# Performance work log

Hardware: AMD Instinct MI355X
Metric: run time of the kernel (lower is better)

## Reference

```python
import jax, jax.numpy as jnp
import numpy as np

EMB = 768
HEADS = 12
HEAD_DIM = EMB // HEADS
LN_EPS = 1e-5


def _layernorm(x, g, b):
    mu = jnp.mean(x, axis=-1, keepdims=True)
    var = jnp.mean(jnp.square(x - mu), axis=-1, keepdims=True)
    return (x - mu) * jax.lax.rsqrt(var + LN_EPS) * g + b


def _att_block(x, ln_g, ln_b, w_qkv, b_qkv, w_proj, b_proj):
    # x: [b, n, e]
    B, N, E = x.shape
    h, d = HEADS, HEAD_DIM
    qkv = _layernorm(x, ln_g, ln_b) @ w_qkv.T + b_qkv          # [b, n, 3e]
    # einops 'b n (h d qkv)': last axis factors as (h, d, 3), qkv innermost
    qkv = qkv.reshape(B, N, h, d, 3)
    qkv = jnp.moveaxis(qkv, (4, 2), (0, 2))                    # [3, b, h, n, d]
    q, k, v = qkv[0], qkv[1], qkv[2]
    scale = d ** (-0.5)
    # NOTE: original code DIVIDES by scale (= multiplies by sqrt(d)) -- faithful
    scores = jnp.einsum('bhqd,bhkd->bhqk', q, k) / scale       # [b, h, n, n]
    attn = jax.nn.softmax(scores, axis=-1)
    out = jnp.einsum('bhqk,bhkd->bhqd', attn, v)               # [b, h, n, d]
    out = out.transpose(0, 2, 1, 3).reshape(B, N, E)           # [b, n, e]
    return x + out @ w_proj.T + b_proj


def setup_inputs() -> dict:
    key = jax.random.key(0)
    ks = jax.random.split(key, 8)
    B, N, E = 2, 2048, EMB
    s = E ** (-0.5)
    return {
        'modal1': jax.random.normal(ks[0], (B, N, E), jnp.float32),
        'modal2': jax.random.normal(ks[1], (B, N, E), jnp.float32),
        'ln1_g': jnp.ones((E,), jnp.float32),
        'ln1_b': jnp.zeros((E,), jnp.float32),
        'w_qkv1': jax.random.normal(ks[2], (3 * E, E), jnp.float32) * s,
        'b_qkv1': jnp.zeros((3 * E,), jnp.float32),
        'w_proj1': jax.random.normal(ks[3], (E, E), jnp.float32) * s,
        'b_proj1': jnp.zeros((E,), jnp.float32),
        'ln2_g': jnp.ones((E,), jnp.float32),
        'ln2_b': jnp.zeros((E,), jnp.float32),
        'w_qkv2': jax.random.normal(ks[4], (3 * E, E), jnp.float32) * s,
        'b_qkv2': jnp.zeros((3 * E,), jnp.float32),
        'w_proj2': jax.random.normal(ks[5], (E, E), jnp.float32) * s,
        'b_proj2': jnp.zeros((E,), jnp.float32),
    }


def reference(modal1, modal2, ln1_g, ln1_b, w_qkv1, b_qkv1, w_proj1, b_proj1,
              ln2_g, ln2_b, w_qkv2, b_qkv2, w_proj2, b_proj2):
    out1 = _att_block(modal1, ln1_g, ln1_b, w_qkv1, b_qkv1, w_proj1, b_proj1)
    out2 = _att_block(modal2, ln2_g, ln2_b, w_qkv2, b_qkv2, w_proj2, b_proj2)
    return (out1, out2)
```

## Files before the change

### kernel.cpp

```cpp
#include <hip/hip_runtime.h>
#include <hip/hip_bf16.h>


typedef unsigned short u16;
typedef unsigned int   u32;
typedef __attribute__((ext_vector_type(4)))  float floatx4;
typedef __attribute__((ext_vector_type(16))) float floatx16;
typedef __attribute__((ext_vector_type(8)))  short shortx8;
typedef __attribute__((ext_vector_type(2)))  unsigned int uintx2;

#define EMB   768
#define SEQ   2048
#define NHEAD 12
#define HDIM  64
#define RPM   4096
#define NROW  8192
#define NUNIT 48
#define LDA   40
#define KTS   4096

__device__ __forceinline__ float bf2f(u16 h) {
  union { u32 u; float f; } v; v.u = ((u32)h) << 16; return v.f;
}
__device__ __forceinline__ u16 f2bf(float f) {
  union { float f; u32 u; } v; v.f = f;
  u32 r = v.u + 0x7fffu + ((v.u >> 16) & 1u);
  return (u16)(r >> 16);
}
__device__ __forceinline__ u32 cvtpk_bf16(float a, float b) {
  u32 r;
  asm("v_cvt_pk_bf16_f32 %0, %1, %2" : "=v"(r) : "v"(a), "v"(b));
  return r;
}
__device__ __forceinline__ void swap_halves(u32 a, u32 b, u32& x, u32& y) {
#if __has_builtin(__builtin_amdgcn_permlane32_swap)
  uintx2 r = __builtin_amdgcn_permlane32_swap(a, b, false, false);
  x = r.x; y = r.y;
#else
  u32 ax = (u32)__shfl_xor((int)a, 32);
  u32 bx = (u32)__shfl_xor((int)b, 32);
  bool h = (threadIdx.x & 32) != 0;
  x = h ? bx : a;
  y = h ? b : ax;
#endif
}

__global__ __launch_bounds__(256) void prep_wq(
    const float* __restrict__ wq1, const float* __restrict__ wq2,
    u16* __restrict__ wh, u16* __restrict__ wl)
{
  int bx = blockIdx.x;
  int modal = bx / 2304, rowp = bx % 2304;
  int typ = rowp / 768, hd = rowp % 768;
  const float* W = (modal ? wq2 : wq1) + (size_t)(hd * 3 + typ) * EMB;
  size_t dst = (size_t)bx * EMB;
  int t = threadIdx.x;
  #pragma unroll
  for (int i = 0; i < 3; ++i) {
    int e = t + i * 256;
    float v = W[e];
    u16 h = f2bf(v);
    wh[dst + e] = h;
    wl[dst + e] = f2bf(v - bf2f(h));
  }
}

__global__ __launch_bounds__(256) void prep_wp(
    const float* __restrict__ wp1, const float* __restrict__ wp2,
    u16* __restrict__ wh)
{
  int bx = blockIdx.x;
  int modal = bx / 768, row = bx % 768;
  const float* W = (modal ? wp2 : wp1) + (size_t)row * EMB;
  size_t dst = (size_t)bx * EMB;
  int t = threadIdx.x;
  #pragma unroll
  for (int i = 0; i < 3; ++i) {
    int e = t + i * 256;
    wh[dst + e] = f2bf(W[e]);
  }
}

__global__ __launch_bounds__(256) void k_ln(
    const float* __restrict__ x1, const float* __restrict__ x2,
    const float* __restrict__ g1, const float* __restrict__ b1,
    const float* __restrict__ g2, const float* __restrict__ b2,
    u16* __restrict__ xn_hi, u16* __restrict__ xn_lo)
{
  int row = blockIdx.x;
  int modal = row >> 12;
  const float* x = modal ? x2 : x1;
  const float* g = modal ? g2 : g1;
  const float* bb = modal ? b2 : b1;
  int r = row & (RPM - 1);
  const float* xr = x + (size_t)r * EMB;
  int t = threadIdx.x;
  float v0 = xr[t], v1 = xr[t + 256], v2 = xr[t + 512];
  float s = v0 + v1 + v2;
  float s2 = v0 * v0 + v1 * v1 + v2 * v2;
  #pragma unroll
  for (int m = 1; m < 64; m <<= 1) { s += __shfl_xor(s, m); s2 += __shfl_xor(s2, m); }
  __shared__ float ls[4], ls2[4];
  int w = t >> 6;
  if ((t & 63) == 0) { ls[w] = s; ls2[w] = s2; }
  __syncthreads();
  s = ls[0] + ls[1] + ls[2] + ls[3];
  s2 = ls2[0] + ls2[1] + ls2[2] + ls2[3];
  float mu = s * (1.0f / EMB);
  float var = s2 * (1.0f / EMB) - mu * mu;
  float rs = rsqrtf(var + 1e-5f);
  size_t base = (size_t)row * EMB;
  float vv[3] = { v0, v1, v2 };
  #pragma unroll
  for (int i = 0; i < 3; ++i) {
    int e = t + i * 256;
    float xn = (vv[i] - mu) * rs * g[e] + bb[e];
    u16 h = f2bf(xn);
    xn_hi[base + e] = h;
    xn_lo[base + e] = f2bf(xn - bf2f(h));
  }
}

__global__ __launch_bounds__(256) void k_qkv(
    const u16* __restrict__ xn_hi, const u16* __restrict__ xn_lo,
    const u16* __restrict__ wqh, const u16* __restrict__ wql,
    const float* __restrict__ bq1, const float* __restrict__ bq2,
    u16* __restrict__ q_hi, u16* __restrict__ q_lo,
    u16* __restrict__ k_hi, u16* __restrict__ k_lo,
    u16* __restrict__ vT)
{
  int mt = blockIdx.x, ntile = blockIdx.y, modal = blockIdx.z;
  const float* BQ = modal ? bq2 : bq1;
  int typ = ntile / 6;
  int hd0 = (ntile % 6) * 128;

  __shared__ u16 As_hi[128 * LDA], As_lo[128 * LDA], Wh[128 * LDA], Wl[128 * LDA];

  int tid = threadIdx.x, lane = tid & 63, w = tid >> 6;
  int wm = (w >> 1) * 64, wn = (w & 1) * 64;
  int lc = lane & 15, lq = lane >> 4;

  floatx4 acc[4][4] = {};
  size_t arow0 = (size_t)(modal * RPM + mt * 128) * EMB;
  size_t wrow0 = (size_t)(modal * 2304 + typ * 768 + hd0) * EMB;

  for (int k0 = 0; k0 < EMB; k0 += 32) {
    #pragma unroll
    for (int i = 0; i < 2; ++i) {
      int c = tid + i * 256;
      int rr = c >> 2, cc = (c & 3) * 8;
      size_t go = (size_t)rr * EMB + k0 + cc;
      *(shortx8*)&As_hi[rr * LDA + cc] = *(const shortx8*)(xn_hi + arow0 + go);
      *(shortx8*)&Wh[rr * LDA + cc]    = *(const shortx8*)(wqh + wrow0 + go);
      if (typ != 2) {
        *(shortx8*)&As_lo[rr * LDA + cc] = *(const shortx8*)(xn_lo + arow0 + go);
        *(shortx8*)&Wl[rr * LDA + cc]    = *(const shortx8*)(wql + wrow0 + go);
      }
    }
    __syncthreads();
    shortx8 ah[4], al[4], wh[4], wl[4];
    #pragma unroll
    for (int i = 0; i < 4; ++i) {
      ah[i] = *(const shortx8*)&As_hi[(wm + i * 16 + lc) * LDA + lq * 8];
      wh[i] = *(const shortx8*)&Wh[(wn + i * 16 + lc) * LDA + lq * 8];
      if (typ != 2) {
        al[i] = *(const shortx8*)&As_lo[(wm + i * 16 + lc) * LDA + lq * 8];
        wl[i] = *(const shortx8*)&Wl[(wn + i * 16 + lc) * LDA + lq * 8];
      }
    }
    #pragma unroll
    for (int i = 0; i < 4; ++i)
      #pragma unroll
      for (int jn = 0; jn < 4; ++jn) {
        acc[i][jn] = __builtin_amdgcn_mfma_f32_16x16x32_bf16(ah[i], wh[jn], acc[i][jn], 0, 0, 0);
        if (typ != 2) {
          acc[i][jn] = __builtin_amdgcn_mfma_f32_16x16x32_bf16(al[i], wh[jn], acc[i][jn], 0, 0, 0);
          acc[i][jn] = __builtin_amdgcn_mfma_f32_16x16x32_bf16(ah[i], wl[jn], acc[i][jn], 0, 0, 0);
        }
      }
    __syncthreads();
  }

  #pragma unroll
  for (int i = 0; i < 4; ++i) {
    int mrow0 = mt * 128 + wm + i * 16 + lq * 4;
    #pragma unroll
    for (int jn = 0; jn < 4; ++jn) {
      int colp = hd0 + wn + jn * 16 + lc;
      int h = colp >> 6, d = colp & 63;
      float bias = BQ[colp * 3 + typ];
      #pragma unroll
      for (int r = 0; r < 4; ++r) {
        int mrow = mrow0 + r;
        int b = mrow >> 11, nq = mrow & (SEQ - 1);
        int uu = modal * 24 + b * 12 + h;
        float val = acc[i][jn][r] + bias;
        if (typ == 0) {
          size_t o = ((size_t)uu * SEQ + nq) * HDIM + d;
          u16 hh = f2bf(val); q_hi[o] = hh; q_lo[o] = f2bf(val - bf2f(hh));
        } else if (typ == 1) {
          size_t o = ((size_t)uu * SEQ + nq) * HDIM + d;
          u16 hh = f2bf(val); k_hi[o] = hh; k_lo[o] = f2bf(val - bf2f(hh));
        } else {
          vT[((size_t)uu * HDIM + d) * SEQ + nq] = f2bf(val);
        }
      }
    }
  }
}

__global__ __launch_bounds__(256, 3) void k_attn(
    const u16* __restrict__ q_hi, const u16* __restrict__ q_lo,
    const u16* __restrict__ k_hi, const u16* __restrict__ k_lo,
    const u16* __restrict__ vT, u16* __restrict__ attn_out)
{
  int qt = blockIdx.x, u = blockIdx.y;
  __shared__ u16 lds[2][3 * KTS];

  int tid = threadIdx.x, lane = tid & 63, w = tid >> 6;
  int col = lane & 31, hi = lane >> 5;
  int swz = (col & 7) << 4;

  shortx8 qh[4], qlo[4];
  {
    size_t qb = ((size_t)u * SEQ + qt * 128 + w * 32 + col) * HDIM + hi * 8;
    #pragma unroll
    for (int s = 0; s < 4; ++s) {
      qh[s]  = *(const shortx8*)(q_hi + qb + s * 16);
      qlo[s] = *(const shortx8*)(q_lo + qb + s * 16);
    }
  }

  int lrow = lane >> 3;
  int lcol = ((lane & 7) ^ lrow) << 3;
  const u16* kh_src = k_hi + (size_t)u * SEQ * HDIM;
  const u16* kl_src = k_lo + (size_t)u * SEQ * HDIM;
  const u16* v_src  = vT  + (size_t)u * HDIM * SEQ;

  auto stage = [&](int buf, int kc) {
    #pragma unroll
    for (int c = 0; c < 6; ++c) {
      int seg = w * 6 + c;
      int tile = seg >> 3, segin = seg & 7;
      u16* dst = &lds[buf][tile * KTS + segin * 512];
      const u16* src;
      if (tile == 0)      src = kh_src + (size_t)(kc + segin * 8 + lrow) * HDIM + lcol;
      else if (tile == 1) src = kl_src + (size_t)(kc + segin * 8 + lrow) * HDIM + lcol;
      else                src = v_src  + (size_t)(segin * 8 + lrow) * SEQ + kc + lcol;
      __builtin_amdgcn_global_load_lds(
          (const __attribute__((address_space(1))) unsigned int*)src,
          (__attribute__((address_space(3))) unsigned int*)dst, 16, 0, 0);
    }
  };

  floatx16 O0 = {}, O1 = {};
  float m_r = -1e30f, lsum = 0.0f;
  const float Cs = 11.5415603271f;
  const float THR = 8.0f;

  stage(0, 0);
  __syncthreads();

  for (int t = 0; t < SEQ / 64; ++t) {
    int cur = t & 1;
    if (t + 1 < SEQ / 64) stage(cur ^ 1, (t + 1) * 64);

    const char* Kh = (const char*)&lds[cur][0];
    const char* Kl = (const char*)&lds[cur][KTS];
    const char* Vt = (const char*)&lds[cur][2 * KTS];

    floatx16 S0 = {}, S1 = {};
    __builtin_amdgcn_s_setprio(1);
    #pragma unroll
    for (int s = 0; s < 4; ++s) {
      int cb = (s * 32 + hi * 16) ^ swz;
      shortx8 kf0 = *(const shortx8*)(Kh + col * 128 + cb);
      shortx8 kl0 = *(const shortx8*)(Kl + col * 128 + cb);
      shortx8 kf1 = *(const shortx8*)(Kh + (32 + col) * 128 + cb);
      shortx8 kl1 = *(const shortx8*)(Kl + (32 + col) * 128 + cb);
      S0 = __builtin_amdgcn_mfma_f32_32x32x16_bf16(kf0, qh[s],  S0, 0, 0, 0);
      S1 = __builtin_amdgcn_mfma_f32_32x32x16_bf16(kf1, qh[s],  S1, 0, 0, 0);
      S0 = __builtin_amdgcn_mfma_f32_32x32x16_bf16(kf0, qlo[s], S0, 0, 0, 0);
      S1 = __builtin_amdgcn_mfma_f32_32x32x16_bf16(kf1, qlo[s], S1, 0, 0, 0);
      S0 = __builtin_amdgcn_mfma_f32_32x32x16_bf16(kl0, qh[s],  S0, 0, 0, 0);
      S1 = __builtin_amdgcn_mfma_f32_32x32x16_bf16(kl1, qh[s],  S1, 0, 0, 0);
    }
    __builtin_amdgcn_s_setprio(0);

    float tm[16];
    #pragma unroll
    for (int r = 0; r < 16; ++r) tm[r] = fmaxf(S0[r], S1[r]);
    #pragma unroll
    for (int st = 8; st >= 1; st >>= 1)
      #pragma unroll
      for (int i = 0; i < st; ++i) tm[i] = fmaxf(tm[i], tm[i + st]);
    float mx = tm[0] * Cs;
    mx = fmaxf(mx, __shfl_xor(mx, 32));

    if (!__all(mx <= m_r + THR)) {
      float mn = fmaxf(m_r, mx);
      float alpha = __builtin_amdgcn_exp2f(m_r - mn);
      m_r = mn;
      lsum *= alpha;
      #pragma unroll
      for (int r = 0; r < 16; ++r) {
        int qsrc = (r & 3) + 8 * (r >> 2) + 4 * hi;
        union { float f; int i; } a; a.f = alpha;
        a.i = __builtin_amdgcn_ds_bpermute(qsrc << 2, a.i);
        O0[r] *= a.f; O1[r] *= a.f;
      }
    }

    #pragma unroll
    for (int r = 0; r < 16; ++r) {
      S0[r] = __builtin_amdgcn_exp2f(fmaf(Cs, S0[r], -m_r));
      S1[r] = __builtin_amdgcn_exp2f(fmaf(Cs, S1[r], -m_r));
    }
    #pragma unroll
    for (int r = 0; r < 16; ++r) tm[r] = S0[r] + S1[r];
    #pragma unroll
    for (int st = 8; st >= 1; st >>= 1)
      #pragma unroll
      for (int i = 0; i < st; ++i) tm[i] += tm[i + st];
    lsum += tm[0];

    shortx8 pf[4];
    #pragma unroll
    for (int kt = 0; kt < 2; ++kt)
      #pragma unroll
      for (int h2 = 0; h2 < 2; ++h2) {
        floatx16 Sv = kt ? S1 : S0;
        int b0 = h2 * 8;
        u32 A = cvtpk_bf16(Sv[b0 + 0], Sv[b0 + 1]);
        u32 B = cvtpk_bf16(Sv[b0 + 2], Sv[b0 + 3]);
        u32 C = cvtpk_bf16(Sv[b0 + 4], Sv[b0 + 5]);
        u32 D = cvtpk_bf16(Sv[b0 + 6], Sv[b0 + 7]);
        u32 w0, w1, w2, w3;
        swap_halves(A, C, w0, w2);
        swap_halves(B, D, w1, w3);
        union { u32 uu[4]; shortx8 ss; } pk_;
        pk_.uu[0] = w0; pk_.uu[1] = w1; pk_.uu[2] = w2; pk_.uu[3] = w3;
        pf[kt * 2 + h2] = pk_.ss;
      }

    __builtin_amdgcn_s_setprio(1);
    #pragma unroll
    for (int ks = 0; ks < 4; ++ks) {
      int cb = (ks * 32 + hi * 16) ^ swz;
      shortx8 v0 = *(const shortx8*)(Vt + col * 128 + cb);
      shortx8 v1 = *(const shortx8*)(Vt + (32 + col) * 128 + cb);
      O0 = __builtin_amdgcn_mfma_f32_32x32x16_bf16(pf[ks], v0, O0, 0, 0, 0);
      O1 = __builtin_amdgcn_mfma_f32_32x32x16_bf16(pf[ks], v1, O1, 0, 0, 0);
    }
    __builtin_amdgcn_s_setprio(0);

    __syncthreads();
  }

  float lt = lsum + __shfl_xor(lsum, 32);
  float rl = __builtin_amdgcn_rcpf(lt);
  int modal = u / 24, b = (u / 12) & 1, h = u % 12;
  size_t obase = ((size_t)(modal * RPM + b * SEQ + qt * 128 + w * 32)) * EMB + h * 64 + col;
  #pragma unroll
  for (int r = 0; r < 16; ++r) {
    int ql_ = (r & 3) + 8 * (r >> 2) + 4 * hi;
    union { float f; int i; } a; a.f = rl;
    a.i = __builtin_amdgcn_ds_bpermute(ql_ << 2, a.i);
    size_t ob = obase + (size_t)ql_ * EMB;
    attn_out[ob]      = f2bf(O0[r] * a.f);
    attn_out[ob + 32] = f2bf(O1[r] * a.f);
  }
}

__global__ __launch_bounds__(256) void k_proj(
    const u16* __restrict__ ao, const u16* __restrict__ wph,
    const float* __restrict__ x1, const float* __restrict__ x2,
    const float* __restrict__ bp1, const float* __restrict__ bp2,
    float* __restrict__ out)
{
  int mt = blockIdx.x, ntile = blockIdx.y, modal = blockIdx.z;
  const float* BP = modal ? bp2 : bp1;
  const float* x  = modal ? x2 : x1;

  __shared__ u16 As[128 * LDA], Ws[128 * LDA];
  int tid = threadIdx.x, lane = tid & 63, w = tid >> 6;
  int wm = (w >> 1) * 64, wn = (w & 1) * 64;
  int lc = lane & 15, lq = lane >> 4;

  floatx4 acc[4][4] = {};
  size_t arow0 = (size_t)(modal * RPM + mt * 128) * EMB;
  int col0 = ntile * 128;
  size_t wrow0 = (size_t)(modal * 768 + col0) * EMB;

  for (int k0 = 0; k0 < EMB; k0 += 32) {
    #pragma unroll
    for (int i = 0; i < 2; ++i) {
      int c = tid + i * 256;
      int rr = c >> 2, cc = (c & 3) * 8;
      size_t go = (size_t)rr * EMB + k0 + cc;
      *(shortx8*)&As[rr * LDA + cc] = *(const shortx8*)(ao + arow0 + go);
      *(shortx8*)&Ws[rr * LDA + cc] = *(const shortx8*)(wph + wrow0 + go);
    }
    __syncthreads();
    shortx8 af[4], wf[4];
    #pragma unroll
    for (int i = 0; i < 4; ++i) {
      af[i] = *(const shortx8*)&As[(wm + i * 16 + lc) * LDA + lq * 8];
      wf[i] = *(const shortx8*)&Ws[(wn + i * 16 + lc) * LDA + lq * 8];
    }
    #pragma unroll
    for (int i = 0; i < 4; ++i)
      #pragma unroll
      for (int jn = 0; jn < 4; ++jn)
        acc[i][jn] = __builtin_amdgcn_mfma_f32_16x16x32_bf16(af[i], wf[jn], acc[i][jn], 0, 0, 0);
    __syncthreads();
  }

  #pragma unroll
  for (int i = 0; i < 4; ++i) {
    int mrow0 = mt * 128 + wm + i * 16 + lq * 4;
    #pragma unroll
    for (int jn = 0; jn < 4; ++jn) {
      int col = col0 + wn + jn * 16 + lc;
      float bias = BP[col];
      #pragma unroll
      for (int r = 0; r < 4; ++r) {
        int mrow = mrow0 + r;
        float val = acc[i][jn][r] + bias + x[(size_t)mrow * EMB + col];
        out[((size_t)(modal * RPM + mrow)) * EMB + col] = val;
      }
    }
  }
}

extern "C" void kernel_launch(void* const* d_in, const int* in_sizes, int n_in,
                              void* d_out, int out_size, void* d_ws, size_t ws_size,
                              hipStream_t stream) {
  const float* modal1 = (const float*)d_in[0];
  const float* modal2 = (const float*)d_in[1];
  const float* ln1_g  = (const float*)d_in[2];
  const float* ln1_b  = (const float*)d_in[3];
  const float* w_qkv1 = (const float*)d_in[4];
  const float* b_qkv1 = (const float*)d_in[5];
  const float* w_proj1= (const float*)d_in[6];
  const float* b_proj1= (const float*)d_in[7];
  const float* ln2_g  = (const float*)d_in[8];
  const float* ln2_b  = (const float*)d_in[9];
  const float* w_qkv2 = (const float*)d_in[10];
  const float* b_qkv2 = (const float*)d_in[11];
  const float* w_proj2= (const float*)d_in[12];
  const float* b_proj2= (const float*)d_in[13];
  float* out = (float*)d_out;

  const size_t BUFE = (size_t)NROW * EMB;
  const size_t WQE  = (size_t)2 * 2304 * EMB;
  u16* xn_hi = (u16*)d_ws;
  u16* xn_lo = xn_hi + BUFE;
  u16* q_hi  = xn_lo + BUFE;
  u16* q_lo  = q_hi + BUFE;
  u16* k_hi  = q_lo + BUFE;
  u16* k_lo  = k_hi + BUFE;
  u16* vT    = k_lo + BUFE;
  u16* wq_h  = vT + BUFE;
  u16* wq_l  = wq_h + WQE;
  u16* attn  = xn_hi;
  u16* wp_h  = q_lo;

  prep_wq<<<4608, 256, 0, stream>>>(w_qkv1, w_qkv2, wq_h, wq_l);
  k_ln<<<NROW, 256, 0, stream>>>(modal1, modal2, ln1_g, ln1_b, ln2_g, ln2_b, xn_hi, xn_lo);
  dim3 g2(32, 18, 2);
  k_qkv<<<g2, 256, 0, stream>>>(xn_hi, xn_lo, wq_h, wq_l, b_qkv1, b_qkv2,
                                q_hi, q_lo, k_hi, k_lo, vT);
  dim3 g3(16, 48);
  k_attn<<<g3, 256, 0, stream>>>(q_hi, q_lo, k_hi, k_lo, vT, attn);
  prep_wp<<<1536, 256, 0, stream>>>(w_proj1, w_proj2, wp_h);
  dim3 g4(32, 6, 2);
  k_proj<<<g4, 256, 0, stream>>>(attn, wp_h, modal1, modal2, b_proj1, b_proj2, out);
}
```

Before: 357.2 us.

## Double query rows per attention wave and use async LDS loads in QKV GEMM

The attention kernel now has each wave process two 32-row query groups against the same staged K/V tile. Each block covers 256 queries, the grid halves, and every K/V LDS fragment read is reused across twice as many MFMAs. This raises register pressure, so occupancy drops to 2 blocks per CU and only 384 blocks fill the device. The QKV GEMM switches from register-staged global-to-LDS copies to global_load_lds with an XOR-swizzled unpadded layout, and it skips the lo-part loads for V tiles.

```diff
diff --git a/kernel.cpp b/kernel.cpp
--- a/kernel.cpp
+++ b/kernel.cpp
@@ -134,48 +134,74 @@
   int typ = ntile / 6;
   int hd0 = (ntile % 6) * 128;
 
-  __shared__ u16 As_hi[128 * LDA], As_lo[128 * LDA], Wh[128 * LDA], Wl[128 * LDA];
+  __shared__ __align__(16) u16 As_hi[128 * 32], Wh[128 * 32], As_lo[128 * 32], Wl[128 * 32];
 
   int tid = threadIdx.x, lane = tid & 63, w = tid >> 6;
   int wm = (w >> 1) * 64, wn = (w & 1) * 64;
   int lc = lane & 15, lq = lane >> 4;
 
+  int srow = lane >> 2;
+  int schunk = ((lane & 3) ^ (srow & 3)) << 3;
+
   floatx4 acc[4][4] = {};
-  size_t arow0 = (size_t)(modal * RPM + mt * 128) * EMB;
-  size_t wrow0 = (size_t)(modal * 2304 + typ * 768 + hd0) * EMB;
+  const u16* aH = xn_hi + (size_t)(modal * RPM + mt * 128) * EMB;
+  const u16* aL = xn_lo + (size_t)(modal * RPM + mt * 128) * EMB;
+  const u16* wH = wqh + (size_t)(modal * 2304 + typ * 768 + hd0) * EMB;
+  const u16* wL = wql + (size_t)(modal * 2304 + typ * 768 + hd0) * EMB;
 
   for (int k0 = 0; k0 < EMB; k0 += 32) {
-    #pragma unroll
-    for (int i = 0; i < 2; ++i) {
-      int c = tid + i * 256;
-      int rr = c >> 2, cc = (c & 3) * 8;
-      size_t go = (size_t)rr * EMB + k0 + cc;
-      *(shortx8*)&As_hi[rr * LDA + cc] = *(const shortx8*)(xn_hi + arow0 + go);
-      *(shortx8*)&Wh[rr * LDA + cc]    = *(const shortx8*)(wqh + wrow0 + go);
+    if (typ != 2) {
+      #pragma unroll
+      for (int c = 0; c < 8; ++c) {
+        int seg = w * 8 + c;
+        int tile = seg >> 3, segin = seg & 7;
+        size_t off = (size_t)(segin * 16 + srow) * EMB + k0 + schunk;
+        const u16* src; u16* dstb;
+        if (tile == 0)      { src = aH + off; dstb = As_hi; }
+        else if (tile == 1) { src = wH + off; dstb = Wh; }
+        else if (tile == 2) { src = aL + off; dstb = As_lo; }
+        else                { src = wL + off; dstb = Wl; }
+        __builtin_amdgcn_global_load_lds(
+            (const __attribute__((address_space(1))) unsigned int*)src,
+            (__attribute__((address_space(3))) unsigned int*)(dstb + segin * 512), 16, 0, 0);
+      }
+    } else {
+      #pragma unroll
+      for (int c = 0; c < 4; ++c) {
+        int seg = w * 4 + c;
+        int tile = seg >> 3, segin = seg & 7;
+        size_t off = (size_t)(segin * 16 + srow) * EMB + k0 + schunk;
+        const u16* src; u16* dstb;
+        if (tile == 0) { src = aH + off; dstb = As_hi; }
+        else           { src = wH + off; dstb = Wh; }
+        __builtin_amdgcn_global_load_lds(
+            (const __attribute__((address_space(1))) unsigned int*)src,
+            (__attribute__((address_space(3))) unsigned int*)(dstb + segin * 512), 16, 0, 0);
+      }
+    }
+    __syncthreads();
+
+    shortx8 ah[4], al[4], whf[4], wlf[4];
+    int rsw = lc & 3;
+    int ca = (lq ^ rsw) << 3;
+    #pragma unroll
+    for (int i = 0; i < 4; ++i) {
+      int ra = wm + i * 16 + lc, rw = wn + i * 16 + lc;
+      ah[i]  = *(const shortx8*)&As_hi[ra * 32 + ca];
+      whf[i] = *(const shortx8*)&Wh[rw * 32 + ca];
       if (typ != 2) {
-        *(shortx8*)&As_lo[rr * LDA + cc] = *(const shortx8*)(xn_lo + arow0 + go);
-        *(shortx8*)&Wl[rr * LDA + cc]    = *(const shortx8*)(wql + wrow0 + go);
-      }
-    }
-    __syncthreads();
-    shortx8 ah[4], al[4], wh[4], wl[4];
-    #pragma unroll
-    for (int i = 0; i < 4; ++i) {
-      ah[i] = *(const shortx8*)&As_hi[(wm + i * 16 + lc) * LDA + lq * 8];
-      wh[i] = *(const shortx8*)&Wh[(wn + i * 16 + lc) * LDA + lq * 8];
-      if (typ != 2) {
-        al[i] = *(const shortx8*)&As_lo[(wm + i * 16 + lc) * LDA + lq * 8];
-        wl[i] = *(const shortx8*)&Wl[(wn + i * 16 + lc) * LDA + lq * 8];
+        al[i]  = *(const shortx8*)&As_lo[ra * 32 + ca];
+        wlf[i] = *(const shortx8*)&Wl[rw * 32 + ca];
       }
     }
     #pragma unroll
     for (int i = 0; i < 4; ++i)
       #pragma unroll
       for (int jn = 0; jn < 4; ++jn) {
-        acc[i][jn] = __builtin_amdgcn_mfma_f32_16x16x32_bf16(ah[i], wh[jn], acc[i][jn], 0, 0, 0);
+        acc[i][jn] = __builtin_amdgcn_mfma_f32_16x16x32_bf16(ah[i], whf[jn], acc[i][jn], 0, 0, 0);
         if (typ != 2) {
-          acc[i][jn] = __builtin_amdgcn_mfma_f32_16x16x32_bf16(al[i], wh[jn], acc[i][jn], 0, 0, 0);
-          acc[i][jn] = __builtin_amdgcn_mfma_f32_16x16x32_bf16(ah[i], wl[jn], acc[i][jn], 0, 0, 0);
+          acc[i][jn] = __builtin_amdgcn_mfma_f32_16x16x32_bf16(al[i], whf[jn], acc[i][jn], 0, 0, 0);
+          acc[i][jn] = __builtin_amdgcn_mfma_f32_16x16x32_bf16(ah[i], wlf[jn], acc[i][jn], 0, 0, 0);
         }
       }
     __syncthreads();
@@ -209,25 +235,26 @@
   }
 }
 
-__global__ __launch_bounds__(256, 3) void k_attn(
+__global__ __launch_bounds__(256, 2) void k_attn(
     const u16* __restrict__ q_hi, const u16* __restrict__ q_lo,
     const u16* __restrict__ k_hi, const u16* __restrict__ k_lo,
     const u16* __restrict__ vT, u16* __restrict__ attn_out)
 {
   int qt = blockIdx.x, u = blockIdx.y;
-  __shared__ u16 lds[2][3 * KTS];
+  __shared__ __align__(16) u16 lds[2][3 * KTS];
 
   int tid = threadIdx.x, lane = tid & 63, w = tid >> 6;
   int col = lane & 31, hi = lane >> 5;
   int swz = (col & 7) << 4;
 
-  shortx8 qh[4], qlo[4];
-  {
-    size_t qb = ((size_t)u * SEQ + qt * 128 + w * 32 + col) * HDIM + hi * 8;
+  shortx8 qh[2][4], qlo[2][4];
+  #pragma unroll
+  for (int g = 0; g < 2; ++g) {
+    size_t qb = ((size_t)u * SEQ + qt * 256 + w * 64 + g * 32 + col) * HDIM + hi * 8;
     #pragma unroll
     for (int s = 0; s < 4; ++s) {
-      qh[s]  = *(const shortx8*)(q_hi + qb + s * 16);
-      qlo[s] = *(const shortx8*)(q_lo + qb + s * 16);
+      qh[g][s]  = *(const shortx8*)(q_hi + qb + s * 16);
+      qlo[g][s] = *(const shortx8*)(q_lo + qb + s * 16);
     }
   }
 
@@ -253,8 +280,9 @@
     }
   };
 
-  floatx16 O0 = {}, O1 = {};
-  float m_r = -1e30f, lsum = 0.0f;
+  floatx16 O[2][2] = {};
+  float m_r[2] = { -1e30f, -1e30f };
+  float lsum[2] = { 0.0f, 0.0f };
   const float Cs = 11.5415603271f;
   const float THR = 8.0f;
 
@@ -269,79 +297,87 @@
     const char* Kl = (const char*)&lds[cur][KTS];
     const char* Vt = (const char*)&lds[cur][2 * KTS];
 
-    floatx16 S0 = {}, S1 = {};
+    floatx16 S0[2] = {}, S1[2] = {};
     __builtin_amdgcn_s_setprio(1);
     #pragma unroll
     for (int s = 0; s < 4; ++s) {
       int cb = (s * 32 + hi * 16) ^ swz;
       shortx8 kf0 = *(const shortx8*)(Kh + col * 128 + cb);
-      shortx8 kl0 = *(const shortx8*)(Kl + col * 128 + cb);
+      shortx8 kc0 = *(const shortx8*)(Kl + col * 128 + cb);
       shortx8 kf1 = *(const shortx8*)(Kh + (32 + col) * 128 + cb);
-      shortx8 kl1 = *(const shortx8*)(Kl + (32 + col) * 128 + cb);
-      S0 = __builtin_amdgcn_mfma_f32_32x32x16_bf16(kf0, qh[s],  S0, 0, 0, 0);
-      S1 = __builtin_amdgcn_mfma_f32_32x32x16_bf16(kf1, qh[s],  S1, 0, 0, 0);
-      S0 = __builtin_amdgcn_mfma_f32_32x32x16_bf16(kf0, qlo[s], S0, 0, 0, 0);
-      S1 = __builtin_amdgcn_mfma_f32_32x32x16_bf16(kf1, qlo[s], S1, 0, 0, 0);
-      S0 = __builtin_amdgcn_mfma_f32_32x32x16_bf16(kl0, qh[s],  S0, 0, 0, 0);
-      S1 = __builtin_amdgcn_mfma_f32_32x32x16_bf16(kl1, qh[s],  S1, 0, 0, 0);
+      shortx8 kc1 = *(const shortx8*)(Kl + (32 + col) * 128 + cb);
+      #pragma unroll
+      for (int g = 0; g < 2; ++g) {
+        S0[g] = __builtin_amdgcn_mfma_f32_32x32x16_bf16(kf0, qh[g][s],  S0[g], 0, 0, 0);
+        S1[g] = __builtin_amdgcn_mfma_f32_32x32x16_bf16(kf1, qh[g][s],  S1[g], 0, 0, 0);
+        S0[g] = __builtin_amdgcn_mfma_f32_32x32x16_bf16(kf0, qlo[g][s], S0[g], 0, 0, 0);
+        S1[g] = __builtin_amdgcn_mfma_f32_32x32x16_bf16(kf1, qlo[g][s], S1[g], 0, 0, 0);
+        S0[g] = __builtin_amdgcn_mfma_f32_32x32x16_bf16(kc0, qh[g][s],  S0[g], 0, 0, 0);
+        S1[g] = __builtin_amdgcn_mfma_f32_32x32x16_bf16(kc1, qh[g][s],  S1[g], 0, 0, 0);
+      }
     }
     __builtin_amdgcn_s_setprio(0);
 
-    float tm[16];
-    #pragma unroll
-    for (int r = 0; r < 16; ++r) tm[r] = fmaxf(S0[r], S1[r]);
-    #pragma unroll
-    for (int st = 8; st >= 1; st >>= 1)
-      #pragma unroll
-      for (int i = 0; i < st; ++i) tm[i] = fmaxf(tm[i], tm[i + st]);
-    float mx = tm[0] * Cs;
-    mx = fmaxf(mx, __shfl_xor(mx, 32));
-
-    if (!__all(mx <= m_r + THR)) {
-      float mn = fmaxf(m_r, mx);
-      float alpha = __builtin_amdgcn_exp2f(m_r - mn);
-      m_r = mn;
-      lsum *= alpha;
+    shortx8 pf[2][4];
+    #pragma unroll
+    for (int g = 0; g < 2; ++g) {
+      float tm[16];
+      #pragma unroll
+      for (int r = 0; r < 16; ++r) tm[r] = fmaxf(S0[g][r], S1[g][r]);
+      float m0 = fmaxf(fmaxf(tm[0], tm[1]), tm[2]);
+      float m1 = fmaxf(fmaxf(tm[3], tm[4]), tm[5]);
+      float m2 = fmaxf(fmaxf(tm[6], tm[7]), tm[8]);
+      float m3 = fmaxf(fmaxf(tm[9], tm[10]), tm[11]);
+      float m4 = fmaxf(fmaxf(tm[12], tm[13]), tm[14]);
+      float mx = fmaxf(fmaxf(fmaxf(m0, m1), m2), fmaxf(fmaxf(m3, m4), tm[15]));
+      mx *= Cs;
+      mx = fmaxf(mx, __shfl_xor(mx, 32));
+
+      if (!__all(mx <= m_r[g] + THR)) {
+        float mn = fmaxf(m_r[g], mx);
+        float alpha = __builtin_amdgcn_exp2f(m_r[g] - mn);
+        m_r[g] = mn;
+        lsum[g] *= alpha;
+        #pragma unroll
+        for (int r = 0; r < 16; ++r) {
+          int qsrc = (r & 3) + 8 * (r >> 2) + 4 * hi;
+          union { float f; int i; } a; a.f = alpha;
+          a.i = __builtin_amdgcn_ds_bpermute(qsrc << 2, a.i);
+          O[g][0][r] *= a.f; O[g][1][r] *= a.f;
+        }
+      }
+
       #pragma unroll
       for (int r = 0; r < 16; ++r) {
-        int qsrc = (r & 3) + 8 * (r >> 2) + 4 * hi;
-        union { float f; int i; } a; a.f = alpha;
-        a.i = __builtin_amdgcn_ds_bpermute(qsrc << 2, a.i);
-        O0[r] *= a.f; O1[r] *= a.f;
-      }
-    }
-
-    #pragma unroll
-    for (int r = 0; r < 16; ++r) {
-      S0[r] = __builtin_amdgcn_exp2f(fmaf(Cs, S0[r], -m_r));
-      S1[r] = __builtin_amdgcn_exp2f(fmaf(Cs, S1[r], -m_r));
-    }
-    #pragma unroll
-    for (int r = 0; r < 16; ++r) tm[r] = S0[r] + S1[r];
-    #pragma unroll
-    for (int st = 8; st >= 1; st >>= 1)
-      #pragma unroll
-      for (int i = 0; i < st; ++i) tm[i] += tm[i + st];
-    lsum += tm[0];
-
-    shortx8 pf[4];
-    #pragma unroll
-    for (int kt = 0; kt < 2; ++kt)
-      #pragma unroll
-      for (int h2 = 0; h2 < 2; ++h2) {
-        floatx16 Sv = kt ? S1 : S0;
-        int b0 = h2 * 8;
-        u32 A = cvtpk_bf16(Sv[b0 + 0], Sv[b0 + 1]);
-        u32 B = cvtpk_bf16(Sv[b0 + 2], Sv[b0 + 3]);
-        u32 C = cvtpk_bf16(Sv[b0 + 4], Sv[b0 + 5]);
-        u32 D = cvtpk_bf16(Sv[b0 + 6], Sv[b0 + 7]);
-        u32 w0, w1, w2, w3;
-        swap_halves(A, C, w0, w2);
-        swap_halves(B, D, w1, w3);
-        union { u32 uu[4]; shortx8 ss; } pk_;
-        pk_.uu[0] = w0; pk_.uu[1] = w1; pk_.uu[2] = w2; pk_.uu[3] = w3;
-        pf[kt * 2 + h2] = pk_.ss;
-      }
+        S0[g][r] = __builtin_amdgcn_exp2f(fmaf(Cs, S0[g][r], -m_r[g]));
+        S1[g][r] = __builtin_amdgcn_exp2f(fmaf(Cs, S1[g][r], -m_r[g]));
+      }
+      #pragma unroll
+      for (int r = 0; r < 16; ++r) tm[r] = S0[g][r] + S1[g][r];
+      #pragma unroll
+      for (int st = 8; st >= 1; st >>= 1)
+        #pragma unroll
+        for (int i = 0; i < st; ++i) tm[i] += tm[i + st];
+      lsum[g] += tm[0];
+
+      #pragma unroll
+      for (int kt = 0; kt < 2; ++kt)
+        #pragma unroll
+        for (int h2 = 0; h2 < 2; ++h2) {
+          floatx16 Sv = kt ? S1[g] : S0[g];
+          int b0 = h2 * 8;
+          u32 A = cvtpk_bf16(Sv[b0 + 0], Sv[b0 + 1]);
+          u32 B = cvtpk_bf16(Sv[b0 + 2], Sv[b0 + 3]);
+          u32 C = cvtpk_bf16(Sv[b0 + 4], Sv[b0 + 5]);
+          u32 D = cvtpk_bf16(Sv[b0 + 6], Sv[b0 + 7]);
+          u32 w0, w1, w2, w3;
+          swap_halves(A, C, w0, w2);
+          swap_halves(B, D, w1, w3);
+          union { u32 uu[4]; shortx8 ss; } pk_;
+          pk_.uu[0] = w0; pk_.uu[1] = w1; pk_.uu[2] = w2; pk_.uu[3] = w3;
+          pf[g][kt * 2 + h2] = pk_.ss;
+        }
+    }
 
     __builtin_amdgcn_s_setprio(1);
     #pragma unroll
@@ -349,26 +385,33 @@
       int cb = (ks * 32 + hi * 16) ^ swz;
       shortx8 v0 = *(const shortx8*)(Vt + col * 128 + cb);
       shortx8 v1 = *(const shortx8*)(Vt + (32 + col) * 128 + cb);
-      O0 = __builtin_amdgcn_mfma_f32_32x32x16_bf16(pf[ks], v0, O0, 0, 0, 0);
-      O1 = __builtin_amdgcn_mfma_f32_32x32x16_bf16(pf[ks], v1, O1, 0, 0, 0);
+      #pragma unroll
+      for (int g = 0; g < 2; ++g) {
+        O[g][0] = __builtin_amdgcn_mfma_f32_32x32x16_bf16(pf[g][ks], v0, O[g][0], 0, 0, 0);
+        O[g][1] = __builtin_amdgcn_mfma_f32_32x32x16_bf16(pf[g][ks], v1, O[g][1], 0, 0, 0);
+      }
     }
     __builtin_amdgcn_s_setprio(0);
 
     __syncthreads();
   }
 
-  float lt = lsum + __shfl_xor(lsum, 32);
-  float rl = __builtin_amdgcn_rcpf(lt);
   int modal = u / 24, b = (u / 12) & 1, h = u % 12;
-  size_t obase = ((size_t)(modal * RPM + b * SEQ + qt * 128 + w * 32)) * EMB + h * 64 + col;
-  #pragma unroll
-  for (int r = 0; r < 16; ++r) {
-    int ql_ = (r & 3) + 8 * (r >> 2) + 4 * hi;
-    union { float f; int i; } a; a.f = rl;
-    a.i = __builtin_amdgcn_ds_bpermute(ql_ << 2, a.i);
-    size_t ob = obase + (size_t)ql_ * EMB;
-    attn_out[ob]      = f2bf(O0[r] * a.f);
-    attn_out[ob + 32] = f2bf(O1[r] * a.f);
+  #pragma unroll
+  for (int g = 0; g < 2; ++g) {
+    float lt = lsum[g] + __shfl_xor(lsum[g], 32);
+    float rl = __builtin_amdgcn_rcpf(lt);
+    size_t obase = ((size_t)(modal * RPM + b * SEQ + qt * 256 + w * 64 + g * 32)) * EMB
+                 + h * 64 + col;
+    #pragma unroll
+    for (int r = 0; r < 16; ++r) {
+      int ql_ = (r & 3) + 8 * (r >> 2) + 4 * hi;
+      union { float f; int i; } a; a.f = rl;
+      a.i = __builtin_amdgcn_ds_bpermute(ql_ << 2, a.i);
+      size_t ob = obase + (size_t)ql_ * EMB;
+      attn_out[ob]      = f2bf(O[g][0][r] * a.f);
+      attn_out[ob + 32] = f2bf(O[g][1][r] * a.f);
+    }
   }
 }
 
@@ -471,7 +514,7 @@
   dim3 g2(32, 18, 2);
   k_qkv<<<g2, 256, 0, stream>>>(xn_hi, xn_lo, wq_h, wq_l, b_qkv1, b_qkv2,
                                 q_hi, q_lo, k_hi, k_lo, vT);
-  dim3 g3(16, 48);
+  dim3 g3(8, 48);
   k_attn<<<g3, 256, 0, stream>>>(q_hi, q_lo, k_hi, k_lo, vT, attn);
   prep_wp<<<1536, 256, 0, stream>>>(w_proj1, w_proj2, wp_h);
   dim3 g4(32, 6, 2);
```

Result: slower. 444.2 us (+24.4%).

## Use direct global-to-LDS loads with XOR swizzle in GEMMs, remap attention blocks per XCD

Applied to the files above, without the earlier changes.

The QKV and projection GEMMs now load tiles with global_load_lds straight into an unpadded, XOR-swizzled LDS layout instead of going through registers into padded LDS. The projection kernel drops to 64-row tiles and doubles its grid, which gives more blocks to fill the CUs. The attention kernel remaps block IDs so that all query tiles of a head land on the same XCD, which should improve L2 reuse of K and V. Together these aim to cut the load-instruction and register cost of staging tiles and to raise cache locality. They add swizzle indexing complexity, and the smaller projection tile gives less reuse per block.

```diff
diff --git a/kernel.cpp b/kernel.cpp
--- a/kernel.cpp
+++ b/kernel.cpp
@@ -16,7 +16,6 @@
 #define RPM   4096
 #define NROW  8192
 #define NUNIT 48
-#define LDA   40
 #define KTS   4096
 
 __device__ __forceinline__ float bf2f(u16 h) {
@@ -134,48 +133,74 @@
   int typ = ntile / 6;
   int hd0 = (ntile % 6) * 128;
 
-  __shared__ u16 As_hi[128 * LDA], As_lo[128 * LDA], Wh[128 * LDA], Wl[128 * LDA];
+  __shared__ __align__(16) u16 As_hi[128 * 32], Wh[128 * 32], As_lo[128 * 32], Wl[128 * 32];
 
   int tid = threadIdx.x, lane = tid & 63, w = tid >> 6;
   int wm = (w >> 1) * 64, wn = (w & 1) * 64;
   int lc = lane & 15, lq = lane >> 4;
 
+  int srow = lane >> 2;
+  int schunk = ((lane & 3) ^ (srow & 3)) << 3;
+
   floatx4 acc[4][4] = {};
-  size_t arow0 = (size_t)(modal * RPM + mt * 128) * EMB;
-  size_t wrow0 = (size_t)(modal * 2304 + typ * 768 + hd0) * EMB;
+  const u16* aH = xn_hi + (size_t)(modal * RPM + mt * 128) * EMB;
+  const u16* aL = xn_lo + (size_t)(modal * RPM + mt * 128) * EMB;
+  const u16* wH = wqh + (size_t)(modal * 2304 + typ * 768 + hd0) * EMB;
+  const u16* wL = wql + (size_t)(modal * 2304 + typ * 768 + hd0) * EMB;
 
   for (int k0 = 0; k0 < EMB; k0 += 32) {
-    #pragma unroll
-    for (int i = 0; i < 2; ++i) {
-      int c = tid + i * 256;
-      int rr = c >> 2, cc = (c & 3) * 8;
-      size_t go = (size_t)rr * EMB + k0 + cc;
-      *(shortx8*)&As_hi[rr * LDA + cc] = *(const shortx8*)(xn_hi + arow0 + go);
-      *(shortx8*)&Wh[rr * LDA + cc]    = *(const shortx8*)(wqh + wrow0 + go);
+    if (typ != 2) {
+      #pragma unroll
+      for (int c = 0; c < 8; ++c) {
+        int seg = w * 8 + c;
+        int tile = seg >> 3, segin = seg & 7;
+        size_t off = (size_t)(segin * 16 + srow) * EMB + k0 + schunk;
+        const u16* src; u16* dstb;
+        if (tile == 0)      { src = aH + off; dstb = As_hi; }
+        else if (tile == 1) { src = wH + off; dstb = Wh; }
+        else if (tile == 2) { src = aL + off; dstb = As_lo; }
+        else                { src = wL + off; dstb = Wl; }
+        __builtin_amdgcn_global_load_lds(
+            (const __attribute__((address_space(1))) unsigned int*)src,
+            (__attribute__((address_space(3))) unsigned int*)(dstb + segin * 512), 16, 0, 0);
+      }
+    } else {
+      #pragma unroll
+      for (int c = 0; c < 4; ++c) {
+        int seg = w * 4 + c;
+        int tile = seg >> 3, segin = seg & 7;
+        size_t off = (size_t)(segin * 16 + srow) * EMB + k0 + schunk;
+        const u16* src; u16* dstb;
+        if (tile == 0) { src = aH + off; dstb = As_hi; }
+        else           { src = wH + off; dstb = Wh; }
+        __builtin_amdgcn_global_load_lds(
+            (const __attribute__((address_space(1))) unsigned int*)src,
+            (__attribute__((address_space(3))) unsigned int*)(dstb + segin * 512), 16, 0, 0);
+      }
+    }
+    __syncthreads();
+
+    shortx8 ah[4], al[4], whf[4], wlf[4];
+    int rsw = lc & 3;
+    int ca = (lq ^ rsw) << 3;
+    #pragma unroll
+    for (int i = 0; i < 4; ++i) {
+      int ra = wm + i * 16 + lc, rw = wn + i * 16 + lc;
+      ah[i]  = *(const shortx8*)&As_hi[ra * 32 + ca];
+      whf[i] = *(const shortx8*)&Wh[rw * 32 + ca];
       if (typ != 2) {
-        *(shortx8*)&As_lo[rr * LDA + cc] = *(const shortx8*)(xn_lo + arow0 + go);
-        *(shortx8*)&Wl[rr * LDA + cc]    = *(const shortx8*)(wql + wrow0 + go);
-      }
-    }
-    __syncthreads();
-    shortx8 ah[4], al[4], wh[4], wl[4];
-    #pragma unroll
-    for (int i = 0; i < 4; ++i) {
-      ah[i] = *(const shortx8*)&As_hi[(wm + i * 16 + lc) * LDA + lq * 8];
-      wh[i] = *(const shortx8*)&Wh[(wn + i * 16 + lc) * LDA + lq * 8];
-      if (typ != 2) {
-        al[i] = *(const shortx8*)&As_lo[(wm + i * 16 + lc) * LDA + lq * 8];
-        wl[i] = *(const shortx8*)&Wl[(wn + i * 16 + lc) * LDA + lq * 8];
+        al[i]  = *(const shortx8*)&As_lo[ra * 32 + ca];
+        wlf[i] = *(const shortx8*)&Wl[rw * 32 + ca];
       }
     }
     #pragma unroll
     for (int i = 0; i < 4; ++i)
       #pragma unroll
       for (int jn = 0; jn < 4; ++jn) {
-        acc[i][jn] = __builtin_amdgcn_mfma_f32_16x16x32_bf16(ah[i], wh[jn], acc[i][jn], 0, 0, 0);
+        acc[i][jn] = __builtin_amdgcn_mfma_f32_16x16x32_bf16(ah[i], whf[jn], acc[i][jn], 0, 0, 0);
         if (typ != 2) {
-          acc[i][jn] = __builtin_amdgcn_mfma_f32_16x16x32_bf16(al[i], wh[jn], acc[i][jn], 0, 0, 0);
-          acc[i][jn] = __builtin_amdgcn_mfma_f32_16x16x32_bf16(ah[i], wl[jn], acc[i][jn], 0, 0, 0);
+          acc[i][jn] = __builtin_amdgcn_mfma_f32_16x16x32_bf16(al[i], whf[jn], acc[i][jn], 0, 0, 0);
+          acc[i][jn] = __builtin_amdgcn_mfma_f32_16x16x32_bf16(ah[i], wlf[jn], acc[i][jn], 0, 0, 0);
         }
       }
     __syncthreads();
@@ -214,8 +239,12 @@
     const u16* __restrict__ k_hi, const u16* __restrict__ k_lo,
     const u16* __restrict__ vT, u16* __restrict__ attn_out)
 {
-  int qt = blockIdx.x, u = blockIdx.y;
-  __shared__ u16 lds[2][3 * KTS];
+  int id = blockIdx.x + (blockIdx.y << 4);
+  int xcd = id & 7, j = id >> 3;
+  int u = xcd * 6 + (j >> 4);
+  int qt = j & 15;
+
+  __shared__ __align__(16) u16 lds[2][3 * KTS];
 
   int tid = threadIdx.x, lane = tid & 63, w = tid >> 6;
   int col = lane & 31, hi = lane >> 5;
@@ -382,34 +411,45 @@
   const float* BP = modal ? bp2 : bp1;
   const float* x  = modal ? x2 : x1;
 
-  __shared__ u16 As[128 * LDA], Ws[128 * LDA];
+  __shared__ __align__(16) u16 As[64 * 32], Ws[128 * 32];
   int tid = threadIdx.x, lane = tid & 63, w = tid >> 6;
-  int wm = (w >> 1) * 64, wn = (w & 1) * 64;
+  int wm = (w >> 1) * 32, wn = (w & 1) * 64;
   int lc = lane & 15, lq = lane >> 4;
 
-  floatx4 acc[4][4] = {};
-  size_t arow0 = (size_t)(modal * RPM + mt * 128) * EMB;
-  int col0 = ntile * 128;
-  size_t wrow0 = (size_t)(modal * 768 + col0) * EMB;
+  int srow = lane >> 2;
+  int schunk = ((lane & 3) ^ (srow & 3)) << 3;
+
+  floatx4 acc[2][4] = {};
+  const u16* aP = ao  + (size_t)(modal * RPM + mt * 64) * EMB;
+  const u16* wP = wph + (size_t)(modal * 768 + ntile * 128) * EMB;
 
   for (int k0 = 0; k0 < EMB; k0 += 32) {
     #pragma unroll
-    for (int i = 0; i < 2; ++i) {
-      int c = tid + i * 256;
-      int rr = c >> 2, cc = (c & 3) * 8;
-      size_t go = (size_t)rr * EMB + k0 + cc;
-      *(shortx8*)&As[rr * LDA + cc] = *(const shortx8*)(ao + arow0 + go);
-      *(shortx8*)&Ws[rr * LDA + cc] = *(const shortx8*)(wph + wrow0 + go);
+    for (int c = 0; c < 3; ++c) {
+      int seg = w * 3 + c;
+      const u16* src; u16* dst;
+      if (seg < 4) {
+        src = aP + (size_t)(seg * 16 + srow) * EMB + k0 + schunk;
+        dst = As + seg * 512;
+      } else {
+        int s2 = seg - 4;
+        src = wP + (size_t)(s2 * 16 + srow) * EMB + k0 + schunk;
+        dst = Ws + s2 * 512;
+      }
+      __builtin_amdgcn_global_load_lds(
+          (const __attribute__((address_space(1))) unsigned int*)src,
+          (__attribute__((address_space(3))) unsigned int*)dst, 16, 0, 0);
     }
     __syncthreads();
-    shortx8 af[4], wf[4];
-    #pragma unroll
-    for (int i = 0; i < 4; ++i) {
-      af[i] = *(const shortx8*)&As[(wm + i * 16 + lc) * LDA + lq * 8];
-      wf[i] = *(const shortx8*)&Ws[(wn + i * 16 + lc) * LDA + lq * 8];
-    }
-    #pragma unroll
-    for (int i = 0; i < 4; ++i)
+
+    int ca = (lq ^ (lc & 3)) << 3;
+    shortx8 af[2], wf[4];
+    #pragma unroll
+    for (int i = 0; i < 2; ++i) af[i] = *(const shortx8*)&As[(wm + i * 16 + lc) * 32 + ca];
+    #pragma unroll
+    for (int i = 0; i < 4; ++i) wf[i] = *(const shortx8*)&Ws[(wn + i * 16 + lc) * 32 + ca];
+    #pragma unroll
+    for (int i = 0; i < 2; ++i)
       #pragma unroll
       for (int jn = 0; jn < 4; ++jn)
         acc[i][jn] = __builtin_amdgcn_mfma_f32_16x16x32_bf16(af[i], wf[jn], acc[i][jn], 0, 0, 0);
@@ -417,11 +457,11 @@
   }
 
   #pragma unroll
-  for (int i = 0; i < 4; ++i) {
-    int mrow0 = mt * 128 + wm + i * 16 + lq * 4;
+  for (int i = 0; i < 2; ++i) {
+    int mrow0 = mt * 64 + wm + i * 16 + lq * 4;
     #pragma unroll
     for (int jn = 0; jn < 4; ++jn) {
-      int col = col0 + wn + jn * 16 + lc;
+      int col = ntile * 128 + wn + jn * 16 + lc;
       float bias = BP[col];
       #pragma unroll
       for (int r = 0; r < 4; ++r) {
@@ -474,6 +514,6 @@
   dim3 g3(16, 48);
   k_attn<<<g3, 256, 0, stream>>>(q_hi, q_lo, k_hi, k_lo, vT, attn);
   prep_wp<<<1536, 256, 0, stream>>>(w_proj1, w_proj2, wp_h);
-  dim3 g4(32, 6, 2);
+  dim3 g4(64, 6, 2);
   k_proj<<<g4, 256, 0, stream>>>(attn, wp_h, modal1, modal2, b_proj1, b_proj2, out);
 }
```

New measurement: 355.5 us. Within noise of the previous version (-0.5%).
